# Kernel optimization log

Measured on AMD Instinct MI355X. Metric: run time of the kernel, lower is better.

Reference implementation:

```python
import jax, jax.numpy as jnp
import numpy as np
import math

L_SIDE = 32           # one_side_length = ceil(sqrt(L)), L = 32**2
NDIM = 16             # args.ndim (SSM state size)
N_SSM = 16            # args.n_ssm
DIRS = 4              # args.directions_amount
EMBED = 1024          # embed_dim
KD = DIRS * N_SSM     # kernel_dim = 64
CDIM = EMBED * DIRS   # C_dimensions = 4096
H = EMBED // N_SSM    # 64 (channels per ssm)
R2 = 16               # expansion terms per kernel position
R = L_SIDE * L_SIDE * R2
V = 2 * L_SIDE        # vander power dim (power_dim = kernel_dim_arg*2)
BSZ = 8
SEQ = L_SIDE * L_SIDE


def _build_one_matrix():
    # Mimics CoeffCalculator.whole_as_one: for each of d=2 flow axes and each
    # of R expansion terms, the 4 A-factor rows are one-hot selectors over the
    # V power basis, and the 5th (B) row holds an integer coefficient in one of
    # the first two columns (selecting B1 or B2).
    rng = np.random.default_rng(0)
    M = np.zeros((2, 5, R, V), dtype=np.float32)
    di = np.arange(2)[:, None]
    ri = np.arange(R)[None, :]
    for a in range(4):
        idx = rng.integers(0, V, size=(2, R))
        M[di, a, ri, idx] = 1.0
    col = rng.integers(0, 2, size=(2, R))
    coef = rng.integers(1, 5, size=(2, R)).astype(np.float32)
    M[di, 4, ri, col] = coef
    return jnp.asarray(M)


def setup_inputs() -> dict:
    key = jax.random.key(0)
    ks = jax.random.split(key, 7)
    return {
        "x": jax.random.normal(ks[0], (SEQ, BSZ, EMBED), jnp.float32),
        "A": jax.random.normal(ks[1], (4, KD, NDIM), jnp.float32) * 0.2,
        "B1": jax.random.normal(ks[2], (KD, NDIM), jnp.float32) * 0.2,
        "B2": jax.random.normal(ks[3], (KD, NDIM), jnp.float32) * 0.2,
        "C1": jax.random.normal(ks[4], (CDIM, NDIM), jnp.float32),
        "C2": jax.random.normal(ks[5], (CDIM, NDIM), jnp.float32),
        "omega": jax.random.normal(ks[6], (EMBED,), jnp.float32),
        "one_matrix": _build_one_matrix(),
    }


def _compute_kernel(A, B1, B2, C1, C2, one_matrix, dtype):
    scale = 1.0 / math.sqrt(NDIM)
    # _calc_coeffs: sigmoid on A, B
    As = jax.nn.sigmoid(A)                                  # (4, KD, NDIM)
    pw = jnp.arange(V, dtype=dtype)
    # torch.linalg.vander: increasing powers 0..V-1 -> (4, V, KD, NDIM)
    A_vals = jnp.transpose(As[..., None] ** pw, (0, 3, 1, 2))
    Bs = jax.nn.sigmoid(jnp.stack([B1, B2], 0))             # (2, KD, NDIM)
    Bpad = jnp.zeros((V, KD, NDIM), dtype).at[:2].set(Bs)   # pad to V rows
    vals = jnp.concatenate([A_vals, Bpad[None]], 0)         # (5, V, KD, NDIM)
    # 'd a R V, a V k n -> d a R k n' then product over the 5 factors
    prod = jnp.einsum('drv,vkn->drkn', one_matrix[:, 0], vals[0])
    for a in range(1, 5):
        prod = prod * jnp.einsum('drv,vkn->drkn', one_matrix[:, a], vals[a])
    # sum over r2 expansion terms per kernel position
    w = prod.reshape(2, SEQ, R2, KD, NDIM).sum(2)           # (2, SEQ, KD, NDIM)
    C = jnp.stack([C1, C2], 0) * scale                      # (2, CDIM, NDIM)
    Cr = C.reshape(2, H, KD, NDIM)
    k = jnp.einsum('dpkn,dhkn->phk', w, Cr).reshape(L_SIDE, L_SIDE, CDIM)
    # boundary scaling (first row/col x2, corner net x1)
    k = k.at[0, :, :].multiply(2.0)
    k = k.at[:, 0, :].multiply(2.0)
    k = k.at[0, 0, :].divide(4.0)
    return k


def reference(x, A, B1, B2, C1, C2, omega, one_matrix):
    k = _compute_kernel(A, B1, B2, C1, C2, one_matrix, x.dtype)
    # channel layout (H, dir, n_ssm) -> per-direction (EMBED,) kernels
    kd = k.reshape(L_SIDE, L_SIDE, H, DIRS, N_SSM)
    kd = jnp.transpose(kd, (3, 2, 4, 0, 1)).reshape(DIRS, EMBED, L_SIDE, L_SIDE)
    # 4-corner scans: flip kernel per direction; conv is linear so sum kernels
    ksum = kd[0] + kd[1, :, ::-1, :] + kd[2, :, :, ::-1] + kd[3, :, ::-1, ::-1]
    residual = x * omega                                    # 'L B D, D -> L B D'
    xg = jnp.transpose(x, (1, 2, 0)).reshape(BSZ, EMBED, L_SIDE, L_SIDE)
    s = 2 * L_SIDE
    xf = jnp.fft.rfft2(xg, s=(s, s))                        # (B, D, s, s//2+1)
    kf = jnp.fft.rfft2(ksum, s=(s, s))
    y = jnp.fft.irfft2(xf * kf, s=(s, s))[..., :L_SIDE, :L_SIDE]
    y = jnp.transpose(y.reshape(BSZ, EMBED, SEQ), (2, 0, 1))  # back to (L, B, D)
    return y + residual
```

## Files before the change

kernel.cpp:

```cpp
#include <hip/hip_runtime.h>
#include <stdint.h>


typedef __attribute__((ext_vector_type(8))) short short8;
typedef __attribute__((ext_vector_type(4))) float f32x4;

__device__ inline uint16_t f2bf(float f) {
    uint32_t u = __float_as_uint(f);
    uint32_t r = (u + 0x7FFFu + ((u >> 16) & 1u)) >> 16;
    return (uint16_t)r;
}
__device__ inline float bf2f(uint16_t v) {
    return __uint_as_float((uint32_t)v << 16);
}
__device__ inline uint32_t packbf(float a, float b) {
    return (uint32_t)f2bf(a) | ((uint32_t)f2bf(b) << 16);
}

__global__ __launch_bounds__(256) void k_front2(const float* __restrict__ x,
                                                uint16_t* __restrict__ xtb,
                                                const float* __restrict__ om,
                                                const float* __restrict__ A,
                                                const float* __restrict__ B1,
                                                const float* __restrict__ B2,
                                                float* __restrict__ w) {
    __shared__ __align__(16) float shf[32 * 257];
    int bx = blockIdx.x;
    int t = threadIdx.x;

    if ((bx & 1) == 0) {
        int bi = bx >> 1;
        int u = bi & 31, e0 = (bi >> 5) * 32;
        {
            int c = t & 7, a = t >> 3;
            const float* src = x + (size_t)(u * 256) * 1024 + e0 + c * 4;
            #pragma unroll
            for (int qq = 0; qq < 8; ++qq) {
                int r = qq * 32 + a;
                float4 v = *(const float4*)(src + (size_t)r * 1024);
                shf[(c * 4 + 0) * 257 + r] = v.x;
                shf[(c * 4 + 1) * 257 + r] = v.y;
                shf[(c * 4 + 2) * 257 + r] = v.z;
                shf[(c * 4 + 3) * 257 + r] = v.w;
            }
        }
        __syncthreads();
        {
            int e_local = t >> 3, c = t & 7;
            const float* row = shf + e_local * 257;
            uint16_t* dst = xtb + (size_t)(e0 + e_local) * 8192 + u * 256;
            #pragma unroll
            for (int qq = 0; qq < 4; ++qq) {
                int b = qq * 2 + (c >> 2);
                int v0 = (c & 3) * 8;
                uint32_t pk0 = packbf(row[(v0 + 0) * 8 + b], row[(v0 + 1) * 8 + b]);
                uint32_t pk1 = packbf(row[(v0 + 2) * 8 + b], row[(v0 + 3) * 8 + b]);
                uint32_t pk2 = packbf(row[(v0 + 4) * 8 + b], row[(v0 + 5) * 8 + b]);
                uint32_t pk3 = packbf(row[(v0 + 6) * 8 + b], row[(v0 + 7) * 8 + b]);
                *(uint4*)(dst + b * 32 + v0) = make_uint4(pk0, pk1, pk2, pk3);
            }
        }
    } else {
        int p = bx >> 1;
        float* ffl = shf;
        float* cfl = shf + 128;
        {
            int row_id = t >> 1, h = t & 1;
            int d = row_id >> 6, a = (row_id >> 4) & 3, r2 = row_id & 15;
            const float* src = om + ((size_t)(d * 5 + a) * 16384 + p * 16 + r2) * 64 + h * 32;
            float s = 0.0f;
            #pragma unroll
            for (int q = 0; q < 8; ++q) {
                float4 v = *(const float4*)(src + q * 4);
                float jb = (float)(h * 32 + q * 4);
                s = __builtin_fmaf(v.x, jb,
                    __builtin_fmaf(v.y, jb + 1.0f,
                    __builtin_fmaf(v.z, jb + 2.0f,
                    __builtin_fmaf(v.w, jb + 3.0f, s))));
            }
            s += __shfl_xor(s, 1);
            if (h == 0) ffl[(d * 16 + r2) * 4 + a] = s;
            if (t < 32) {
                int dd = t >> 4, rr = t & 15;
                const float* c = om + ((size_t)(dd * 5 + 4) * 16384 + p * 16 + rr) * 64;
                cfl[(dd * 16 + rr) * 2 + 0] = c[0];
                cfl[(dd * 16 + rr) * 2 + 1] = c[1];
            }
        }

        int d = t >> 7;
        int j0 = (t & 127) * 8;
        float L0[8], L1[8], L2[8], L3[8], B0v[8], B1v[8], acc[8];
        #pragma unroll
        for (int a = 0; a < 4; ++a) {
            float* La = (a == 0) ? L0 : (a == 1) ? L1 : (a == 2) ? L2 : L3;
            float4 u0 = *(const float4*)(A + a * 1024 + j0);
            float4 u1 = *(const float4*)(A + a * 1024 + j0 + 4);
            float tmp[8] = {u0.x, u0.y, u0.z, u0.w, u1.x, u1.y, u1.z, u1.w};
            #pragma unroll
            for (int jj = 0; jj < 8; ++jj)
                La[jj] = -log2f(1.0f + expf(-tmp[jj]));
        }
        {
            float4 u0 = *(const float4*)(B1 + j0);
            float4 u1 = *(const float4*)(B1 + j0 + 4);
            float4 v0 = *(const float4*)(B2 + j0);
            float4 v1 = *(const float4*)(B2 + j0 + 4);
            float t1v[8] = {u0.x, u0.y, u0.z, u0.w, u1.x, u1.y, u1.z, u1.w};
            float t2v[8] = {v0.x, v0.y, v0.z, v0.w, v1.x, v1.y, v1.z, v1.w};
            #pragma unroll
            for (int jj = 0; jj < 8; ++jj) {
                B0v[jj] = 1.0f / (1.0f + expf(-t1v[jj]));
                B1v[jj] = 1.0f / (1.0f + expf(-t2v[jj]));
            }
        }
        #pragma unroll
        for (int jj = 0; jj < 8; ++jj) acc[jj] = 0.0f;
        __syncthreads();

        #pragma unroll
        for (int r2 = 0; r2 < 16; ++r2) {
            float f0 = ffl[(d * 16 + r2) * 4 + 0];
            float f1 = ffl[(d * 16 + r2) * 4 + 1];
            float f2 = ffl[(d * 16 + r2) * 4 + 2];
            float f3 = ffl[(d * 16 + r2) * 4 + 3];
            float c0 = cfl[(d * 16 + r2) * 2 + 0];
            float c1 = cfl[(d * 16 + r2) * 2 + 1];
            #pragma unroll
            for (int jj = 0; jj < 8; ++jj) {
                float ex = __builtin_fmaf(f3, L3[jj],
                           __builtin_fmaf(f2, L2[jj],
                           __builtin_fmaf(f1, L1[jj], f0 * L0[jj])));
                float bs = __builtin_fmaf(c1, B1v[jj], c0 * B0v[jj]);
                acc[jj] = __builtin_fmaf(exp2f(ex), bs, acc[jj]);
            }
        }
        float* dst = w + (size_t)(d * 1024 + p) * 1024 + j0;
        *(float4*)(dst)     = make_float4(acc[0], acc[1], acc[2], acc[3]);
        *(float4*)(dst + 4) = make_float4(acc[4], acc[5], acc[6], acc[7]);
    }
}

__global__ __launch_bounds__(256) void k_kd(const float* __restrict__ w,
                                            const float* __restrict__ C1,
                                            const float* __restrict__ C2,
                                            uint16_t* __restrict__ kd4b) {
    __shared__ float Wl[128 * 33];
    __shared__ float Ctl[32 * 65];
    int kap = blockIdx.x;
    int p0 = blockIdx.y * 128;
    int dir = kap >> 4, m = kap & 15;
    int t = threadIdx.x;

    {
        int off = (t & 3) * 4;
        #pragma unroll
        for (int rep = 0; rep < 4; ++rep) {
            int row_id = rep * 64 + (t >> 2);
            int d = row_id >> 7, pp = row_id & 127;
            const float* src = w + ((size_t)(d * 1024 + p0 + pp) * 64 + kap) * 16 + off;
            float4 v = *(const float4*)src;
            float* dstl = Wl + pp * 33 + d * 16 + off;
            dstl[0] = v.x; dstl[1] = v.y; dstl[2] = v.z; dstl[3] = v.w;
        }
    }
    if (t < 128) {
        int d = t >> 6, h = t & 63;
        const float* Cd = d ? C2 : C1;
        const float* src = Cd + (size_t)(h * 64 + kap) * 16;
        #pragma unroll
        for (int q = 0; q < 16; ++q)
            Ctl[(d * 16 + q) * 65 + h] = src[q] * 0.25f;
    }
    __syncthreads();

    int ph = t & 15, hq = t >> 4;
    int pl = ph * 8, h0 = hq * 4;
    float acc[8][4];
    #pragma unroll
    for (int i = 0; i < 8; ++i)
        { acc[i][0] = acc[i][1] = acc[i][2] = acc[i][3] = 0.0f; }

    for (int k = 0; k < 32; ++k) {
        float c0 = Ctl[k * 65 + h0 + 0];
        float c1 = Ctl[k * 65 + h0 + 1];
        float c2 = Ctl[k * 65 + h0 + 2];
        float c3 = Ctl[k * 65 + h0 + 3];
        #pragma unroll
        for (int i = 0; i < 8; ++i) {
            float wv = Wl[(pl + i) * 33 + k];
            acc[i][0] += wv * c0; acc[i][1] += wv * c1;
            acc[i][2] += wv * c2; acc[i][3] += wv * c3;
        }
    }
    #pragma unroll
    for (int j = 0; j < 4; ++j) {
        int h = h0 + j;
        uint32_t pk[4];
        #pragma unroll
        for (int qq = 0; qq < 4; ++qq) {
            float v0, v1;
            #pragma unroll
            for (int z = 0; z < 2; ++z) {
                int p = p0 + pl + qq * 2 + z;
                int ii = p >> 5, jj = p & 31;
                float f = ((ii == 0) != (jj == 0)) ? 2.0f : 1.0f;
                float val = acc[qq * 2 + z][j] * f;
                if (z == 0) v0 = val; else v1 = val;
            }
            pk[qq] = packbf(v0, v1);
        }
        uint16_t* dst = kd4b + ((size_t)(dir * 1024 + h * 16 + m)) * 1024 + p0 + pl;
        *(uint4*)dst = make_uint4(pk[0], pk[1], pk[2], pk[3]);
    }
}

__global__ __launch_bounds__(256) void k_conv(const uint16_t* __restrict__ xtb,
                                              const uint16_t* __restrict__ kd4b,
                                              uint16_t* __restrict__ ytb) {
    __shared__ __align__(16) char smem[24576 + 16384];
    const int KROW = 768;
    const int SROW = 96;
    char* xtl = smem + 24576;

    int e = blockIdx.x;
    int t = threadIdx.x;
    int lane = t & 63, wv = t >> 6;
    int n = lane & 15, q = lane >> 4, nn = n & 7;

    {
        f32x4 z = {0.f, 0.f, 0.f, 0.f};
        #pragma unroll
        for (int k = 0; k < 6; ++k)
            *(f32x4*)(smem + (t + k * 256) * 16) = z;
    }
    {
        const uint4* src = (const uint4*)(xtb + (size_t)e * 8192);
        #pragma unroll
        for (int r = 0; r < 4; ++r) {
            uint4 v = src[r * 256 + t];
            *(uint4*)(xtl + (r * 256 + t) * 16) = v;
        }
    }
    int pi = t >> 3, pj = (t & 7) * 4;
    float s0, s1, s2, s3;
    {
        const uint16_t* b0 = kd4b + (size_t)e * 1024;
        ushort4 a0 = *(const ushort4*)(b0 + pi * 32 + pj);
        ushort4 a1 = *(const ushort4*)(b0 + (1 << 20) + (31 - pi) * 32 + pj);
        ushort4 a2 = *(const ushort4*)(b0 + (2 << 20) + pi * 32 + (28 - pj));
        ushort4 a3 = *(const ushort4*)(b0 + (3 << 20) + (31 - pi) * 32 + (28 - pj));
        s0 = bf2f(a0.x) + bf2f(a1.x) + bf2f(a2.w) + bf2f(a3.w);
        s1 = bf2f(a0.y) + bf2f(a1.y) + bf2f(a2.z) + bf2f(a3.z);
        s2 = bf2f(a0.z) + bf2f(a1.z) + bf2f(a2.y) + bf2f(a3.y);
        s3 = bf2f(a0.w) + bf2f(a1.w) + bf2f(a2.x) + bf2f(a3.x);
    }
    __syncthreads();

    {
        uint16_t k0 = f2bf(s0), k1 = f2bf(s1), k2 = f2bf(s2), k3 = f2bf(s3);
        #pragma unroll
        for (int s = 0; s < 8; ++s) {
            uint16_t* row = (uint16_t*)(smem + pi * KROW + s * SROW);
            int c = 31 + s - pj;
            row[c]     = k0;
            row[c - 1] = k1;
            row[c - 2] = k2;
            row[c - 3] = k3;
        }
    }
    __syncthreads();

    int A0 = n - 8 * q;
    int A1 = A0 + 16;
    int sh1 = (A1 + 9) & 7;
    int off1 = sh1 * SROW + (31 + sh1 - A1) * 2;
    int off0;
    if (A0 >= -8) {
        int sh0 = (A0 + 9) & 7;
        off0 = sh0 * SROW + (31 + sh0 - A0) * 2;
    } else {
        off0 = 80;
    }
    int boff = nn * 64 + q * 16;

    short8 Breg[16];
    #pragma unroll
    for (int u = 0; u < 16; ++u)
        Breg[u] = *(const short8*)(xtl + u * 512 + boff);

    f32x4 acc0[8], acc1[8];
    #pragma unroll
    for (int ii = 0; ii < 8; ++ii) {
        acc0[ii] = (f32x4){0.f, 0.f, 0.f, 0.f};
        acc1[ii] = (f32x4){0.f, 0.f, 0.f, 0.f};
    }

    #pragma unroll
    for (int dd = 0; dd < 4; ++dd) {
        if (dd <= wv) {
            const char* krow = smem + (wv - dd) * KROW;
            short8 a0 = *(const short8*)(krow + off0);
            short8 a1 = *(const short8*)(krow + off1);
            #pragma unroll
            for (int ii = 0; ii < 8; ++ii) {
                short8 bb = (ii < 4) ? Breg[dd + 4 * ii]
                                     : *(const short8*)(xtl + (dd + 4 * ii) * 512 + boff);
                acc0[ii] = __builtin_amdgcn_mfma_f32_16x16x32_bf16(a0, bb, acc0[ii], 0, 0, 0);
                acc1[ii] = __builtin_amdgcn_mfma_f32_16x16x32_bf16(a1, bb, acc1[ii], 0, 0, 0);
            }
        }
    }
    #pragma unroll
    for (int g = 1; g <= 7; ++g) {
        #pragma unroll
        for (int dd = 0; dd < 4; ++dd) {
            const char* krow = smem + (wv + 4 * g - 3 + dd) * KROW;
            short8 a0 = *(const short8*)(krow + off0);
            short8 a1 = *(const short8*)(krow + off1);
            #pragma unroll
            for (int ii = g; ii < 8; ++ii) {
                int u = 4 * (ii - g) + 3 - dd;
                short8 bb = (ii - g < 4) ? Breg[u]
                                         : *(const short8*)(xtl + u * 512 + boff);
                acc0[ii] = __builtin_amdgcn_mfma_f32_16x16x32_bf16(a0, bb, acc0[ii], 0, 0, 0);
                acc1[ii] = __builtin_amdgcn_mfma_f32_16x16x32_bf16(a1, bb, acc1[ii], 0, 0, 0);
            }
        }
    }

    if (n < 8) {
        uint16_t* base = ytb + ((size_t)(n * 1024 + e)) * 1024 + q * 4;
        #pragma unroll
        for (int ii = 0; ii < 8; ++ii) {
            int i = wv + 4 * ii;
            uint2 w0 = make_uint2(packbf(acc0[ii][0], acc0[ii][1]),
                                  packbf(acc0[ii][2], acc0[ii][3]));
            uint2 w1 = make_uint2(packbf(acc1[ii][0], acc1[ii][1]),
                                  packbf(acc1[ii][2], acc1[ii][3]));
            *(uint2*)(base + i * 32)      = w0;
            *(uint2*)(base + i * 32 + 16) = w1;
        }
    }
}

__global__ __launch_bounds__(256) void k_t2(const uint16_t* __restrict__ ytb,
                                            const float* __restrict__ x,
                                            const float* __restrict__ omega,
                                            float* __restrict__ out) {
    __shared__ float lds[32 * 130];
    int e0 = blockIdx.x * 32, p0 = blockIdx.y * 128, b = blockIdx.z;
    int t = threadIdx.x;
    {
        int a = t >> 3, c = t & 7;
        const uint16_t* src = ytb + (size_t)(b * 1024 + e0 + a) * 1024 + p0;
        float* dst = lds + a * 130;
        #pragma unroll
        for (int rep = 0; rep < 2; ++rep) {
            int off = (c + rep * 8) * 8;
            uint4 v = *(const uint4*)(src + off);
            uint32_t ww[4] = {v.x, v.y, v.z, v.w};
            #pragma unroll
            for (int k = 0; k < 4; ++k) {
                float2 f;
                f.x = bf2f((uint16_t)(ww[k] & 0xFFFFu));
                f.y = bf2f((uint16_t)(ww[k] >> 16));
                *(float2*)(dst + off + k * 2) = f;
            }
        }
    }
    __syncthreads();
    int pl = t >> 1, eh = (t & 1) * 16;
    int p = p0 + pl;
    const float* xs = x + ((size_t)(p * 8 + b)) * 1024 + e0 + eh;
    float* os = out + ((size_t)(p * 8 + b)) * 1024 + e0 + eh;
    #pragma unroll
    for (int qq = 0; qq < 4; ++qq) {
        float4 xv = *(const float4*)(xs + qq * 4);
        int eb = eh + qq * 4;
        float4 ov;
        ov.x = lds[(eb + 0) * 130 + pl] + xv.x * omega[e0 + eb + 0];
        ov.y = lds[(eb + 1) * 130 + pl] + xv.y * omega[e0 + eb + 1];
        ov.z = lds[(eb + 2) * 130 + pl] + xv.z * omega[e0 + eb + 2];
        ov.w = lds[(eb + 3) * 130 + pl] + xv.w * omega[e0 + eb + 3];
        *(float4*)(os + qq * 4) = ov;
    }
}

extern "C" void kernel_launch(void* const* d_in, const int* in_sizes, int n_in,
                              void* d_out, int out_size, void* d_ws, size_t ws_size,
                              hipStream_t stream) {
    (void)in_sizes; (void)n_in; (void)out_size; (void)ws_size;
    const float* x   = (const float*)d_in[0];
    const float* A   = (const float*)d_in[1];
    const float* B1  = (const float*)d_in[2];
    const float* B2  = (const float*)d_in[3];
    const float* C1  = (const float*)d_in[4];
    const float* C2  = (const float*)d_in[5];
    const float* omg = (const float*)d_in[6];
    const float* om  = (const float*)d_in[7];
    float* out = (float*)d_out;

    float* ws  = (float*)d_ws;
    uint16_t* xtb  = (uint16_t*)ws;
    uint16_t* kd4b = (uint16_t*)(ws + 4194304);
    uint16_t* ytb  = (uint16_t*)(ws + 6291456);
    float* w       = ws + 10485760;

    k_front2<<<2048, 256, 0, stream>>>(x, xtb, om, A, B1, B2, w);
    k_kd    <<<dim3(64, 8), 256, 0, stream>>>(w, C1, C2, kd4b);
    k_conv  <<<1024, 256, 0, stream>>>(xtb, kd4b, ytb);
    k_t2    <<<dim3(32, 8, 8), 256, 0, stream>>>(ytb, x, omg, out);
}
```

Before: 199.2 us.

## Restructure conv MFMA loop to pack two output rows per tile and split front transpose

The conv kernel now puts two output rows into each 16-wide MFMA tile, selected by the upper half of the lane's n index. Previously only 8 of 16 columns were used. This halves the accumulator count and drops the preloaded B-register array in favor of a single rolled loop over kernel rows, with zero-pointer reads for out-of-range inputs. The front kernel splits the x transpose into smaller 128-row tiles over 3072 blocks, interleaving two transpose blocks per coefficient block, which halves shared memory per block. The trade-off is more LDS loads per MFMA and a non-unrolled loop with per-iteration branching.

```diff
diff --git a/kernel.cpp b/kernel.cpp
--- a/kernel.cpp
+++ b/kernel.cpp
@@ -17,51 +17,49 @@
     return (uint32_t)f2bf(a) | ((uint32_t)f2bf(b) << 16);
 }
 
-__global__ __launch_bounds__(256) void k_front2(const float* __restrict__ x,
+__global__ __launch_bounds__(256) void k_front3(const float* __restrict__ x,
                                                 uint16_t* __restrict__ xtb,
                                                 const float* __restrict__ om,
                                                 const float* __restrict__ A,
                                                 const float* __restrict__ B1,
                                                 const float* __restrict__ B2,
                                                 float* __restrict__ w) {
-    __shared__ __align__(16) float shf[32 * 257];
+    __shared__ __align__(16) float shf[32 * 129];
     int bx = blockIdx.x;
     int t = threadIdx.x;
-
-    if ((bx & 1) == 0) {
-        int bi = bx >> 1;
-        int u = bi & 31, e0 = (bi >> 5) * 32;
+    int ty = bx % 3;
+
+    if (ty != 2) {
+        int tidx = (bx / 3) * 2 + ty;
+        int u = tidx & 31, e0 = ((tidx >> 5) & 31) * 32, r0 = (tidx >> 10) * 128;
         {
             int c = t & 7, a = t >> 3;
-            const float* src = x + (size_t)(u * 256) * 1024 + e0 + c * 4;
-            #pragma unroll
-            for (int qq = 0; qq < 8; ++qq) {
+            const float* src = x + (size_t)(u * 256 + r0) * 1024 + e0 + c * 4;
+            #pragma unroll
+            for (int qq = 0; qq < 4; ++qq) {
                 int r = qq * 32 + a;
                 float4 v = *(const float4*)(src + (size_t)r * 1024);
-                shf[(c * 4 + 0) * 257 + r] = v.x;
-                shf[(c * 4 + 1) * 257 + r] = v.y;
-                shf[(c * 4 + 2) * 257 + r] = v.z;
-                shf[(c * 4 + 3) * 257 + r] = v.w;
+                shf[(c * 4 + 0) * 129 + r] = v.x;
+                shf[(c * 4 + 1) * 129 + r] = v.y;
+                shf[(c * 4 + 2) * 129 + r] = v.z;
+                shf[(c * 4 + 3) * 129 + r] = v.w;
             }
         }
         __syncthreads();
         {
-            int e_local = t >> 3, c = t & 7;
-            const float* row = shf + e_local * 257;
-            uint16_t* dst = xtb + (size_t)(e0 + e_local) * 8192 + u * 256;
-            #pragma unroll
-            for (int qq = 0; qq < 4; ++qq) {
-                int b = qq * 2 + (c >> 2);
-                int v0 = (c & 3) * 8;
-                uint32_t pk0 = packbf(row[(v0 + 0) * 8 + b], row[(v0 + 1) * 8 + b]);
-                uint32_t pk1 = packbf(row[(v0 + 2) * 8 + b], row[(v0 + 3) * 8 + b]);
-                uint32_t pk2 = packbf(row[(v0 + 4) * 8 + b], row[(v0 + 5) * 8 + b]);
-                uint32_t pk3 = packbf(row[(v0 + 6) * 8 + b], row[(v0 + 7) * 8 + b]);
-                *(uint4*)(dst + b * 32 + v0) = make_uint4(pk0, pk1, pk2, pk3);
-            }
+            int e_local = t >> 3, b = t & 7;
+            const float* row = shf + e_local * 129;
+            int v0 = r0 >> 3;
+            uint32_t pk[8];
+            #pragma unroll
+            for (int k2 = 0; k2 < 8; ++k2)
+                pk[k2] = packbf(row[(2 * k2) * 8 + b], row[(2 * k2 + 1) * 8 + b]);
+            uint16_t* dst = xtb + (size_t)(e0 + e_local) * 8192 + u * 256 + b * 32 + v0;
+            *(uint4*)dst       = make_uint4(pk[0], pk[1], pk[2], pk[3]);
+            *(uint4*)(dst + 8) = make_uint4(pk[4], pk[5], pk[6], pk[7]);
         }
     } else {
-        int p = bx >> 1;
+        int p = bx / 3;
         float* ffl = shf;
         float* cfl = shf + 128;
         {
@@ -226,7 +224,7 @@
     int e = blockIdx.x;
     int t = threadIdx.x;
     int lane = t & 63, wv = t >> 6;
-    int n = lane & 15, q = lane >> 4, nn = n & 7;
+    int n = lane & 15, q = lane >> 4, nn = n & 7, hi = n >> 3;
 
     {
         f32x4 z = {0.f, 0.f, 0.f, 0.f};
@@ -283,63 +281,44 @@
         off0 = 80;
     }
     int boff = nn * 64 + q * 16;
-
-    short8 Breg[16];
+    const char* zptr = smem + 80;
+
+    f32x4 acc0[4], acc1[4];
     #pragma unroll
-    for (int u = 0; u < 16; ++u)
-        Breg[u] = *(const short8*)(xtl + u * 512 + boff);
-
-    f32x4 acc0[8], acc1[8];
-    #pragma unroll
-    for (int ii = 0; ii < 8; ++ii) {
+    for (int ii = 0; ii < 4; ++ii) {
         acc0[ii] = (f32x4){0.f, 0.f, 0.f, 0.f};
         acc1[ii] = (f32x4){0.f, 0.f, 0.f, 0.f};
     }
 
-    #pragma unroll
-    for (int dd = 0; dd < 4; ++dd) {
-        if (dd <= wv) {
-            const char* krow = smem + (wv - dd) * KROW;
-            short8 a0 = *(const short8*)(krow + off0);
-            short8 a1 = *(const short8*)(krow + off1);
-            #pragma unroll
-            for (int ii = 0; ii < 8; ++ii) {
-                short8 bb = (ii < 4) ? Breg[dd + 4 * ii]
-                                     : *(const short8*)(xtl + (dd + 4 * ii) * 512 + boff);
+    int dmax = 2 * wv + 25;
+    for (int di = 0; di <= dmax; ++di) {
+        const char* krow = smem + di * KROW;
+        short8 a0 = *(const short8*)(krow + off0);
+        short8 a1 = *(const short8*)(krow + off1);
+        #pragma unroll
+        for (int ii = 0; ii < 4; ++ii) {
+            int i = 2 * wv + 8 * ii;
+            if (di <= i + 1) {
+                int u = i + hi - di;
+                const char* bp = (u >= 0) ? (xtl + u * 512 + boff) : zptr;
+                short8 bb = *(const short8*)bp;
                 acc0[ii] = __builtin_amdgcn_mfma_f32_16x16x32_bf16(a0, bb, acc0[ii], 0, 0, 0);
                 acc1[ii] = __builtin_amdgcn_mfma_f32_16x16x32_bf16(a1, bb, acc1[ii], 0, 0, 0);
             }
         }
     }
-    #pragma unroll
-    for (int g = 1; g <= 7; ++g) {
-        #pragma unroll
-        for (int dd = 0; dd < 4; ++dd) {
-            const char* krow = smem + (wv + 4 * g - 3 + dd) * KROW;
-            short8 a0 = *(const short8*)(krow + off0);
-            short8 a1 = *(const short8*)(krow + off1);
-            #pragma unroll
-            for (int ii = g; ii < 8; ++ii) {
-                int u = 4 * (ii - g) + 3 - dd;
-                short8 bb = (ii - g < 4) ? Breg[u]
-                                         : *(const short8*)(xtl + u * 512 + boff);
-                acc0[ii] = __builtin_amdgcn_mfma_f32_16x16x32_bf16(a0, bb, acc0[ii], 0, 0, 0);
-                acc1[ii] = __builtin_amdgcn_mfma_f32_16x16x32_bf16(a1, bb, acc1[ii], 0, 0, 0);
-            }
-        }
-    }
-
-    if (n < 8) {
-        uint16_t* base = ytb + ((size_t)(n * 1024 + e)) * 1024 + q * 4;
-        #pragma unroll
-        for (int ii = 0; ii < 8; ++ii) {
-            int i = wv + 4 * ii;
+
+    {
+        uint16_t* base = ytb + ((size_t)(nn * 1024 + e)) * 1024 + q * 4;
+        #pragma unroll
+        for (int ii = 0; ii < 4; ++ii) {
+            int ro = 2 * wv + 8 * ii + hi;
             uint2 w0 = make_uint2(packbf(acc0[ii][0], acc0[ii][1]),
                                   packbf(acc0[ii][2], acc0[ii][3]));
             uint2 w1 = make_uint2(packbf(acc1[ii][0], acc1[ii][1]),
                                   packbf(acc1[ii][2], acc1[ii][3]));
-            *(uint2*)(base + i * 32)      = w0;
-            *(uint2*)(base + i * 32 + 16) = w1;
+            *(uint2*)(base + ro * 32)      = w0;
+            *(uint2*)(base + ro * 32 + 16) = w1;
         }
     }
 }
@@ -407,7 +386,7 @@
     uint16_t* ytb  = (uint16_t*)(ws + 6291456);
     float* w       = ws + 10485760;
 
-    k_front2<<<2048, 256, 0, stream>>>(x, xtb, om, A, B1, B2, w);
+    k_front3<<<3072, 256, 0, stream>>>(x, xtb, om, A, B1, B2, w);
     k_kd    <<<dim3(64, 8), 256, 0, stream>>>(w, C1, C2, kd4b);
     k_conv  <<<1024, 256, 0, stream>>>(xtb, kd4b, ytb);
     k_t2    <<<dim3(32, 8, 8), 256, 0, stream>>>(ytb, x, omg, out);
```

Result: slower. 212.4 us (+6.7%).
